# Performance work log

Hardware: AMD Instinct MI355X
Metric: run time of the kernel (lower is better)

Reference implementation:

```python
import jax, jax.numpy as jnp
import numpy as np
import math

T, B = 512, 32
QD, SD, H, NH = 128, 256, 512, 8
NQ, NS, NSUB = 30000, 400, 8
DKEY = QD + 2 * SD      # 640
DVAL = 4 * SD + QD      # 1152
P = H + 2 * SD + QD     # 1152 (pred_in_feature)
DH = H // NH            # 64
NEG = -1e32


def _layernorm(x, g, b, eps=1e-5):
    mu = jnp.mean(x, axis=-1, keepdims=True)
    var = jnp.mean((x - mu) ** 2, axis=-1, keepdims=True)
    return (x - mu) * jax.lax.rsqrt(var + eps) * g + b


def setup_inputs() -> dict:
    key = jax.random.key(0)
    ks = iter(jax.random.split(key, 48))
    def nrm(shape, scale=0.05):
        return (scale * jax.random.normal(next(ks), shape)).astype(jnp.float32)
    inp = {}
    inp['ans'] = jax.random.randint(next(ks), (T, B), 1, 5, dtype=jnp.int32)
    inp['correct_ans'] = jax.random.randint(next(ks), (T, B), 1, 5, dtype=jnp.int32)
    inp['labels'] = jax.random.randint(next(ks), (T, B), 0, 2, dtype=jnp.int32)
    inp['mask'] = jnp.ones((T, B), jnp.float32)
    inp['q_ids'] = jax.random.randint(next(ks), (T, B), 0, NQ, dtype=jnp.int32)
    inp['subject_ids'] = jax.random.randint(next(ks), (T, B, NSUB), 0, NS, dtype=jnp.int32)
    inp['subject_mask'] = (jax.random.uniform(next(ks), (T, B, NSUB)) < 0.7).astype(jnp.float32)
    inp['Eq'] = nrm((NQ, QD)); inp['Es'] = nrm((NS, SD))
    inp['Ea'] = nrm((4, SD)); inp['El'] = nrm((2, SD))
    inp['Wq'] = nrm((H, DKEY)); inp['bq'] = jnp.zeros((H,), jnp.float32)
    inp['Wk'] = nrm((H, DKEY)); inp['bk'] = jnp.zeros((H,), jnp.float32)
    inp['Wv'] = nrm((H, DVAL)); inp['bv'] = jnp.zeros((H,), jnp.float32)
    inp['Wo'] = nrm((H, H)); inp['bo'] = jnp.zeros((H,), jnp.float32)
    inp['ln1_g'] = jnp.ones((H,), jnp.float32); inp['ln1_b'] = jnp.zeros((H,), jnp.float32)
    inp['W1'] = nrm((H, H)); inp['b1'] = jnp.zeros((H,), jnp.float32)
    inp['W2'] = nrm((H, H)); inp['b2'] = jnp.zeros((H,), jnp.float32)
    inp['ln2_g'] = jnp.ones((H,), jnp.float32); inp['ln2_b'] = jnp.zeros((H,), jnp.float32)
    inp['gammas'] = jnp.zeros((NH, 1, 1), jnp.float32)
    inp['L1W'] = nrm((P, P)); inp['L1b'] = jnp.zeros((P,), jnp.float32)
    inp['L2W'] = nrm((P, P)); inp['L2b'] = jnp.zeros((P,), jnp.float32)
    inp['OW'] = nrm((1, P)); inp['Ob'] = jnp.zeros((1,), jnp.float32)
    return inp


def _forward(ans, correct_ans, labels, q_ids, subject_ids,
             mask, subject_mask, Eq, Es, Ea, El,
             Wq, bq, Wk, bk, Wv, bv, Wo, bo, ln1_g, ln1_b,
             W1, b1, W2, b2, ln2_g, ln2_b, gammas,
             L1W, L1b, L2W, L2b, OW, Ob):
    m3 = mask[:, :, None]                                   # [T,B,1]
    subjects = jnp.sum(Es[subject_ids] * subject_mask[..., None], axis=2)   # [T,B,SD]
    questions = Eq[q_ids]                                   # [T,B,QD]
    ans_embed = Ea[ans - 1] * m3
    ca_embed = Ea[correct_ans - 1]
    lab_embed = El[labels] * m3
    query = jnp.concatenate([questions, subjects, ca_embed], axis=-1)       # [T,B,DKEY]
    value = jnp.concatenate([lab_embed, ans_embed, ca_embed, questions, subjects], axis=-1)  # [T,B,DVAL]
    # note: original applies q_linear to kk and k_linear to qq (qq==kk==query here); akt=True => no pos-embed
    q = (query @ Wq.T + bq).reshape(T, B, NH, DH).transpose(1, 2, 0, 3)     # [B,NH,T,DH]
    k = (query @ Wk.T + bk).reshape(T, B, NH, DH).transpose(1, 2, 0, 3)
    v = (value @ Wv.T + bv).reshape(T, B, NH, DH).transpose(1, 2, 0, 3)
    scores = jnp.einsum('bhqd,bhkd->bhqk', q, k) / math.sqrt(DH)            # [B,NH,T,T]
    scores = jnp.where(mask.T[:, None, None, :] == 0, NEG, scores)
    # exponential distance decay (Softplus-gamma), applied AFTER the key-pad fill as in the original
    idx = jnp.arange(T)
    pe = jnp.sqrt(jnp.abs(idx[None, :] - idx[:, None]).astype(jnp.float32)) # [T,T]
    total_effect = jnp.clip(jnp.exp(pe[None] * (-jax.nn.softplus(gammas))), 1e-5, 1e5)  # [NH,T,T]
    scores = scores * total_effect[None]
    causal_bad = jnp.triu(jnp.ones((T, T), bool))            # upper incl. diagonal is masked
    scores = jnp.where(causal_bad, NEG, scores)
    scores = jax.nn.softmax(scores, axis=-1)
    scores = scores.at[:, :, 0, :].set(0.0)                  # pad-zero first query row
    attn = jnp.einsum('bhqk,bhkd->bhqd', scores, v)
    concat = attn.transpose(2, 0, 1, 3).reshape(T, B, H)
    out = _layernorm(concat @ Wo.T + bo, ln1_g, ln1_b)
    ffn = jax.nn.relu(out @ W1.T + b1) @ W2.T + b2
    out = out + _layernorm(ffn, ln2_g, ln2_b)
    pred = jnp.concatenate([out, questions, subjects, ca_embed], axis=-1)   # [T,B,P]
    h = jax.nn.relu(pred @ L1W.T + L1b)
    h = jax.nn.relu(h @ L2W.T + L2b)
    logits = ((h + pred) @ OW.T + Ob)[..., 0]                # [T,B]
    y = labels.astype(jnp.float32)
    bce = jnp.maximum(logits, 0.0) - logits * y + jnp.log1p(jnp.exp(-jnp.abs(logits)))
    loss = jnp.mean(bce * mask) / jnp.mean(mask)
    return loss


def reference(ans, correct_ans, labels, mask, q_ids, subject_ids, subject_mask,
              Eq, Es, Ea, El, Wq, bq, Wk, bk, Wv, bv, Wo, bo, ln1_g, ln1_b,
              W1, b1, W2, b2, ln2_g, ln2_b, gammas, L1W, L1b, L2W, L2b, OW, Ob):
    return _forward(ans, correct_ans, labels, q_ids, subject_ids,
                    mask, subject_mask, Eq, Es, Ea, El,
                    Wq, bq, Wk, bk, Wv, bv, Wo, bo, ln1_g, ln1_b,
                    W1, b1, W2, b2, ln2_g, ln2_b, gammas,
                    L1W, L1b, L2W, L2b, OW, Ob)
```

## Files before the change

kernel.cpp:

```cpp
#include <hip/hip_runtime.h>
#include <math.h>

#define T_LEN 512
#define B_SZ  32
#define NHEAD 8
#define DHEAD 64
#define H_DIM 512
#define TBTOK 16384
#define P_DIM 1152

typedef unsigned short ushort_t;
typedef short short8 __attribute__((ext_vector_type(8)));
typedef float f32x4 __attribute__((ext_vector_type(4)));

__device__ __forceinline__ ushort_t f2bf(float f) {
    union { float f; unsigned int u; } v; v.f = f;
    unsigned int r = v.u + 0x7fffu + ((v.u >> 16) & 1u);
    return (ushort_t)(r >> 16);
}
__device__ __forceinline__ float bf2f(ushort_t h) {
    union { unsigned int u; float f; } v; v.u = ((unsigned int)h) << 16;
    return v.f;
}
__device__ __forceinline__ void gload_lds16(const void* g, void* l) {
    __builtin_amdgcn_global_load_lds(
        (const __attribute__((address_space(1))) void*)g,
        (__attribute__((address_space(3))) void*)l, 16, 0, 0);
}

__global__ __launch_bounds__(256) void convert_weights(
    const float* __restrict__ wq, const float* __restrict__ wk,
    const float* __restrict__ wv, const float* __restrict__ wo,
    const float* __restrict__ w1, const float* __restrict__ w2,
    const float* __restrict__ l1, const float* __restrict__ l2,
    ushort_t* __restrict__ dst, float* __restrict__ accum)
{
    if (blockIdx.x == 0 && threadIdx.x < 2) accum[threadIdx.x] = 0.f;
    const unsigned int offs[9] = {0u, 327680u, 655360u, 1245184u, 1507328u,
                                  1769472u, 2031616u, 3358720u, 4685824u};
    unsigned int c = (blockIdx.x * 256 + threadIdx.x) * 4;
    const float* srcs[8] = {wq, wk, wv, wo, w1, w2, l1, l2};
    int s = 0;
#pragma unroll
    for (int i = 0; i < 7; i++) s += (c >= offs[i + 1]) ? 1 : 0;
    float4 v = *(const float4*)(srcs[s] + (c - offs[s]));
    ushort4 o;
    o.x = f2bf(v.x); o.y = f2bf(v.y); o.z = f2bf(v.z); o.w = f2bf(v.w);
    *(ushort4*)(dst + c) = o;
}

__global__ __launch_bounds__(256) void embed_kernel(
    const int* __restrict__ ans, const int* __restrict__ cans,
    const int* __restrict__ labels, const float* __restrict__ mask,
    const int* __restrict__ qids, const int* __restrict__ sids,
    const float* __restrict__ smask,
    const float* __restrict__ Eq, const float* __restrict__ Es,
    const float* __restrict__ Ea, const float* __restrict__ El,
    ushort_t* __restrict__ pred_bf, ushort_t* __restrict__ value_bf,
    const float* __restrict__ OW, const float* __restrict__ Ob,
    float* __restrict__ lgits)
{
    __shared__ float red[4];
    int m = blockIdx.x;
    int tid = threadIdx.x;
    float mval = mask[m];
    int qid = qids[m];
    int a   = ans[m] - 1;
    int ca  = cans[m] - 1;
    int lb  = labels[m];
    ushort_t* pr = pred_bf  + (size_t)m * P_DIM;
    ushort_t* vr = value_bf + (size_t)m * P_DIM;

    float part = 0.f;
    if (tid < 128) {
        ushort_t qv = f2bf(Eq[(size_t)qid * 128 + tid]);
        pr[512 + tid] = qv;
        vr[768 + tid] = qv;
        part = bf2f(qv) * OW[512 + tid];
    }
    int d = tid;
    float s = 0.f;
#pragma unroll
    for (int j = 0; j < 8; j++) {
        int  sid = sids[m * 8 + j];
        float sm = smask[m * 8 + j];
        s += Es[(size_t)sid * 256 + d] * sm;
    }
    ushort_t sb = f2bf(s);
    pr[640 + d] = sb;
    vr[896 + d] = sb;
    ushort_t cab = f2bf(Ea[ca * 256 + d]);
    pr[896 + d] = cab;
    vr[512 + d] = cab;
    vr[256 + d] = f2bf(Ea[a * 256 + d] * mval);
    vr[0   + d] = f2bf(El[lb * 256 + d] * mval);

    part = fmaf(bf2f(sb),  OW[640 + d], part);
    part = fmaf(bf2f(cab), OW[896 + d], part);
#pragma unroll
    for (int off = 32; off >= 1; off >>= 1) part += __shfl_xor(part, off, 64);
    if ((tid & 63) == 0) red[tid >> 6] = part;
    __syncthreads();
    if (tid == 0) lgits[m] = red[0] + red[1] + red[2] + red[3] + Ob[0];
}

template<int MODE, bool RELU>
__global__ __launch_bounds__(256) void mgemm(
    const ushort_t* __restrict__ A, int lda,
    const ushort_t* __restrict__ W, int ldw,
    const float* __restrict__ bias, const float* __restrict__ bias2,
    ushort_t* __restrict__ Cb, ushort_t* __restrict__ Cb2, int ldc, int K,
    const float* __restrict__ OW, float* __restrict__ lg)
{
    __shared__ __align__(16) ushort_t As[128 * 32];
    __shared__ __align__(16) ushort_t Ws[128 * 32];
    __shared__ __align__(16) ushort_t et[4][32][72];

    const int m0 = blockIdx.x * 128;
    const int n0 = blockIdx.y * 128;
    const int tid  = threadIdx.x;
    const int wave = tid >> 6;
    const int lane = tid & 63;
    const int wm = wave & 1, wn = wave >> 1;

    f32x4 acc[4][4] = {};

    const int srow = lane >> 2;
    const int lchunk = ((((lane & 3) - ((srow >> 1) & 3)) & 3)) * 8;
    int arowA, arowB;
    if (MODE == 4) {
        int mA = m0 + wave * 32 + srow;
        int mB = mA + 16;
        arowA = ((mA & 511) << 5) + (mA >> 9);
        arowB = ((mB & 511) << 5) + (mB >> 9);
    } else {
        arowA = m0 + wave * 32 + srow;
        arowB = arowA + 16;
    }
    const ushort_t* Ag0 = A + (size_t)arowA * lda + lchunk;
    const ushort_t* Ag1 = A + (size_t)arowB * lda + lchunk;
    const ushort_t* Wg0 = W + (size_t)(n0 + wave * 32 + srow) * ldw + lchunk;
    const ushort_t* Wg1 = Wg0 + (size_t)16 * ldw;
    ushort_t* Al0 = &As[(wave * 32) * 32];
    ushort_t* Al1 = &As[(wave * 32 + 16) * 32];
    ushort_t* Wl0 = &Ws[(wave * 32) * 32];
    ushort_t* Wl1 = &Ws[(wave * 32 + 16) * 32];

    const int fr   = lane & 15;
    const int quad = lane >> 4;
    const int csw  = ((quad + ((fr >> 1) & 3)) & 3) * 8;

    for (int k0 = 0; k0 < K; k0 += 32) {
        gload_lds16(Ag0 + k0, Al0);
        gload_lds16(Ag1 + k0, Al1);
        gload_lds16(Wg0 + k0, Wl0);
        gload_lds16(Wg1 + k0, Wl1);
        __syncthreads();
        short8 af[4], wf[4];
#pragma unroll
        for (int i = 0; i < 4; i++)
            af[i] = *(const short8*)&As[(wm * 64 + i * 16 + fr) * 32 + csw];
#pragma unroll
        for (int j = 0; j < 4; j++)
            wf[j] = *(const short8*)&Ws[(wn * 64 + j * 16 + fr) * 32 + csw];
#pragma unroll
        for (int i = 0; i < 4; i++)
#pragma unroll
            for (int j = 0; j < 4; j++)
                acc[i][j] = __builtin_amdgcn_mfma_f32_16x16x32_bf16(
                    af[i], wf[j], acc[i][j], 0, 0, 0);
        __syncthreads();
    }

    if (MODE == 3) {
#pragma unroll
        for (int i = 0; i < 4; i++)
#pragma unroll
            for (int r = 0; r < 4; r++) {
                int row = m0 + wm * 64 + i * 16 + quad * 4 + r;
                float part = 0.f;
#pragma unroll
                for (int j = 0; j < 4; j++) {
                    int col = n0 + wn * 64 + j * 16 + fr;
                    float v = fmaxf(acc[i][j][r] + bias[col], 0.f);
                    part = fmaf(v, OW[col], part);
                }
                part += __shfl_xor(part, 1, 64);
                part += __shfl_xor(part, 2, 64);
                part += __shfl_xor(part, 4, 64);
                part += __shfl_xor(part, 8, 64);
                if (fr == 0) atomicAdd(&lg[row], part);
            }
        return;
    }

    const int nbase = n0 + wn * 64;
    bool side = (MODE == 5) && (nbase >= 512);
    const float* bp = side ? bias2 : bias;
    const int boff  = (MODE == 5) ? (nbase & 511) : nbase;
    const float scl = (MODE == 5 && !side) ? 0.125f : 1.f;

    const int sub8 = (lane & 7) * 8;
    const int grp  = lane >> 3;

#pragma unroll
    for (int hh = 0; hh < 2; hh++) {
        if (MODE == 4) {
#pragma unroll
            for (int i = 0; i < 4; i++)
#pragma unroll
                for (int r = 0; r < 4; r++) {
                    int rl = i * 16 + quad * 4 + r;
#pragma unroll
                    for (int j = 2 * hh; j < 2 * hh + 2; j++) {
                        int cl = j * 16 + fr;
                        float v = acc[i][j][r] + bp[boff + cl];
                        if (RELU) v = fmaxf(v, 0.f);
                        et[wave][cl - 32 * hh][rl] = f2bf(v);
                    }
                }
        } else {
#pragma unroll
            for (int i = 2 * hh; i < 2 * hh + 2; i++)
#pragma unroll
                for (int r = 0; r < 4; r++) {
                    int rl = i * 16 + quad * 4 + r;
#pragma unroll
                    for (int j = 0; j < 4; j++) {
                        int cl = j * 16 + fr;
                        float v = (acc[i][j][r] + bp[boff + cl]) * scl;
                        if (RELU) v = fmaxf(v, 0.f);
                        et[wave][rl - 32 * hh][cl] = f2bf(v);
                    }
                }
        }
#pragma unroll
        for (int rr = 0; rr < 4; rr++) {
            int rowl = rr * 8 + grp;
            short8 val = *(const short8*)&et[wave][rowl][sub8];
            if (MODE == 1) {
                int row = m0 + wm * 64 + 32 * hh + rowl;
                int col = nbase + sub8;
                *(short8*)&Cb[(size_t)row * ldc + col] = val;
            } else if (MODE == 5) {
                int row = m0 + wm * 64 + 32 * hh + rowl;
                int t = row >> 5, b = row & 31;
                int h = (nbase >> 6) & 7;
                ushort_t* base = side ? Cb2 : Cb;
                *(short8*)&base[(((size_t)(b * 8 + h)) << 15) + ((size_t)t << 6) + sub8] = val;
            } else {
                int m = m0 + wm * 64 + sub8;
                int b = m >> 9, t = m & 511;
                int h = nbase >> 6;
                int d = 32 * hh + rowl;
                *(short8*)&Cb[(((size_t)(b * 8 + h)) << 15) + ((size_t)d << 9) + t] = val;
            }
        }
    }
}

__global__ __launch_bounds__(256) void attn_mfma(
    const ushort_t* __restrict__ qb, const ushort_t* __restrict__ kb,
    const ushort_t* __restrict__ vtb, const float* __restrict__ mask,
    const float* __restrict__ gammas, ushort_t* __restrict__ attnc)
{
    __shared__ __align__(16) ushort_t kbuf[2][64 * 64];
    __shared__ __align__(16) ushort_t vbuf[2][64 * 64];
    __shared__ __align__(16) ushort_t ps[4][16][72];
    __shared__ float decayF[512];
    __shared__ float mneg[512];

    const int bh  = blockIdx.x;
    const int b   = bh >> 3;
    const int h   = bh & 7;
    const int qt0 = (7 - blockIdx.y) * 64;
    const int tid  = threadIdx.x;
    const int wave = tid >> 6;
    const int lane = tid & 63;
    const int fr   = lane & 15;
    const int quad = lane >> 4;

    {
        float g  = gammas[h];
        float sp = (g > 20.f) ? g : log1pf(expf(g));
        for (int i = tid; i < 512; i += 256) {
            decayF[i] = fmaxf(exp2f(-sp * 1.44269504f * sqrtf((float)i)), 1e-5f)
                        * 1.44269504f;
            mneg[i]   = (mask[(size_t)i * B_SZ + b] == 0.f) ? -1e32f : 0.f;
        }
    }

    const int qr0 = qt0 + wave * 16;
    const ushort_t* qbase = qb  + ((size_t)bh << 15);
    const ushort_t* kbase = kb  + ((size_t)bh << 15);
    const ushort_t* vbase = vtb + ((size_t)bh << 15);

    short8 af0 = *(const short8*)(qbase + (size_t)(qr0 + fr) * 64 + quad * 8);
    short8 af1 = *(const short8*)(qbase + (size_t)(qr0 + fr) * 64 + 32 + quad * 8);
    const short8 ones = {0x3F80, 0x3F80, 0x3F80, 0x3F80,
                         0x3F80, 0x3F80, 0x3F80, 0x3F80};

    const int rl0 = wave * 16 + (lane >> 3);
    const int rl1 = rl0 + 8;
    const int sc0 = (((lane & 7) - rl0) & 7) * 8;
    const int sc1 = (((lane & 7) - rl1) & 7) * 8;

    auto stage = [&](int kt, int bufi) {
        gload_lds16(kbase + (size_t)(kt + rl0) * 64 + sc0, &kbuf[bufi][(wave * 16) * 64]);
        gload_lds16(kbase + (size_t)(kt + rl1) * 64 + sc1, &kbuf[bufi][(wave * 16 + 8) * 64]);
        gload_lds16(vbase + (size_t)rl0 * T_LEN + kt + sc0, &vbuf[bufi][(wave * 16) * 64]);
        gload_lds16(vbase + (size_t)rl1 * T_LEN + kt + sc1, &vbuf[bufi][(wave * 16 + 8) * 64]);
    };
    auto frag = [&](const ushort_t* buf, int row, int lchunk) -> short8 {
        return *(const short8*)&buf[row * 64 + ((lchunk + row) & 7) * 8];
    };

    stage(0, 0);

    f32x4 o[4] = {};
    f32x4 lacc = {};
    int bufi = 0;

    for (int kt0 = 0; kt0 <= qt0; kt0 += 64) {
        __syncthreads();
        if (kt0 < qt0) stage(kt0 + 64, bufi ^ 1);
        const bool diag = (kt0 == qt0);
        const ushort_t* kb_ = kbuf[bufi];
        const ushort_t* vb_ = vbuf[bufi];

        f32x4 sacc[4] = {};
#pragma unroll
        for (int j = 0; j < 4; j++) {
            int row = j * 16 + fr;
            short8 k0 = frag(kb_, row, quad);
            short8 k1 = frag(kb_, row, quad + 4);
            sacc[j] = __builtin_amdgcn_mfma_f32_16x16x32_bf16(af0, k0, sacc[j], 0, 0, 0);
            sacc[j] = __builtin_amdgcn_mfma_f32_16x16x32_bf16(af1, k1, sacc[j], 0, 0, 0);
        }

#pragma unroll
        for (int j = 0; j < 4; j++) {
            int kg = kt0 + j * 16 + fr;
            float mn = mneg[kg];
            int qgb = qr0 + quad * 4;
            if (!diag) {
                int base = qgb - kg;
#pragma unroll
                for (int r = 0; r < 4; r++) {
                    float t = fmaf(sacc[j][r], decayF[base + r], mn);
                    union { float f; unsigned u; } cv; cv.f = exp2f(t);
                    ps[wave][quad * 4 + r][j * 16 + fr] = (ushort_t)(cv.u >> 16);
                }
            } else {
#pragma unroll
                for (int r = 0; r < 4; r++) {
                    int didx = qgb + r - kg;
                    float dec = decayF[didx > 0 ? didx : 0];
                    float t = fmaf(sacc[j][r], dec, mn);
                    if (didx <= 0) t = -1e32f;
                    union { float f; unsigned u; } cv; cv.f = exp2f(t);
                    ps[wave][quad * 4 + r][j * 16 + fr] = (ushort_t)(cv.u >> 16);
                }
            }
        }
        short8 pf0 = *(const short8*)&ps[wave][fr][quad * 8];
        short8 pf1 = *(const short8*)&ps[wave][fr][32 + quad * 8];
        lacc = __builtin_amdgcn_mfma_f32_16x16x32_bf16(pf0, ones, lacc, 0, 0, 0);
        lacc = __builtin_amdgcn_mfma_f32_16x16x32_bf16(pf1, ones, lacc, 0, 0, 0);
#pragma unroll
        for (int j2 = 0; j2 < 4; j2++) {
            int row = j2 * 16 + fr;
            short8 v0 = frag(vb_, row, quad);
            short8 v1 = frag(vb_, row, quad + 4);
            o[j2] = __builtin_amdgcn_mfma_f32_16x16x32_bf16(pf0, v0, o[j2], 0, 0, 0);
            o[j2] = __builtin_amdgcn_mfma_f32_16x16x32_bf16(pf1, v1, o[j2], 0, 0, 0);
        }
        bufi ^= 1;
    }

#pragma unroll
    for (int r = 0; r < 4; r++) {
        int qg = qr0 + quad * 4 + r;
        float linv = (qg == 0) ? 0.f : 1.f / lacc[r];
#pragma unroll
        for (int j2 = 0; j2 < 4; j2++)
            ps[wave][quad * 4 + r][j2 * 16 + fr] = f2bf(o[j2][r] * linv);
    }
    const int sub8 = (lane & 7) * 8;
    const int grp  = lane >> 3;
#pragma unroll
    for (int half = 0; half < 2; half++) {
        int rowl = half * 8 + grp;
        short8 val = *(const short8*)&ps[wave][rowl][sub8];
        int qg = qr0 + rowl;
        *(short8*)&attnc[((size_t)qg * B_SZ + b) * H_DIM + h * DHEAD + sub8] = val;
    }
}

__global__ __launch_bounds__(256) void ln1_kernel(
    const ushort_t* __restrict__ X, const float* __restrict__ g,
    const float* __restrict__ bta, ushort_t* __restrict__ Yb)
{
    int m    = blockIdx.x * 4 + (threadIdx.x >> 6);
    int lane = threadIdx.x & 63;
    int c0   = lane * 8;
    const ushort_t* xr = X + (size_t)m * H_DIM + c0;
    float x[8];
    float s = 0.f, ss = 0.f;
    short8 xv = *(const short8*)xr;
#pragma unroll
    for (int i = 0; i < 8; i++) {
        x[i] = bf2f((ushort_t)xv[i]);
        s += x[i]; ss += x[i] * x[i];
    }
#pragma unroll
    for (int off = 32; off >= 1; off >>= 1) {
        s  += __shfl_xor(s,  off, 64);
        ss += __shfl_xor(ss, off, 64);
    }
    float mu  = s * (1.f / 512.f);
    float var = ss * (1.f / 512.f) - mu * mu;
    float rs  = rsqrtf(var + 1e-5f);
    ushort_t yb[8];
#pragma unroll
    for (int i = 0; i < 8; i++)
        yb[i] = f2bf((x[i] - mu) * rs * g[c0 + i] + bta[c0 + i]);
    *(short8*)(Yb + (size_t)m * H_DIM + c0) = *(short8*)&yb[0];
}

__global__ __launch_bounds__(256) void ln2_kernel(
    const ushort_t* __restrict__ X, const float* __restrict__ g,
    const float* __restrict__ bta, const ushort_t* __restrict__ res,
    ushort_t* __restrict__ pred_bf, const float* __restrict__ OW,
    float* __restrict__ lg)
{
    int m    = blockIdx.x * 4 + (threadIdx.x >> 6);
    int lane = threadIdx.x & 63;
    int c0   = lane * 8;
    const ushort_t* xr = X + (size_t)m * H_DIM + c0;
    float x[8];
    float s = 0.f, ss = 0.f;
    short8 xv = *(const short8*)xr;
#pragma unroll
    for (int i = 0; i < 8; i++) {
        x[i] = bf2f((ushort_t)xv[i]);
        s += x[i]; ss += x[i] * x[i];
    }
#pragma unroll
    for (int off = 32; off >= 1; off >>= 1) {
        s  += __shfl_xor(s,  off, 64);
        ss += __shfl_xor(ss, off, 64);
    }
    float mu  = s * (1.f / 512.f);
    float var = ss * (1.f / 512.f) - mu * mu;
    float rs  = rsqrtf(var + 1e-5f);
    short8 rv = *(const short8*)(res + (size_t)m * H_DIM + c0);
    ushort_t yb[8];
    float part = 0.f;
#pragma unroll
    for (int i = 0; i < 8; i++) {
        float v = (x[i] - mu) * rs * g[c0 + i] + bta[c0 + i] + bf2f((ushort_t)rv[i]);
        yb[i] = f2bf(v);
        part = fmaf(v, OW[c0 + i], part);
    }
    *(short8*)(pred_bf + (size_t)m * P_DIM + c0) = *(short8*)&yb[0];
#pragma unroll
    for (int off = 32; off >= 1; off >>= 1) part += __shfl_xor(part, off, 64);
    if (lane == 0) lg[m] += part;
}

__global__ __launch_bounds__(256) void bce_kernel(
    const float* __restrict__ lg, const int* __restrict__ labels,
    const float* __restrict__ mask, float* __restrict__ accum)
{
    int m    = blockIdx.x * 256 + threadIdx.x;
    int lane = threadIdx.x & 63;
    float l  = lg[m];
    float y  = (float)labels[m];
    float mv = mask[m];
    float a  = (fmaxf(l, 0.f) - l * y + log1pf(expf(-fabsf(l)))) * mv;
#pragma unroll
    for (int off = 32; off >= 1; off >>= 1) {
        a  += __shfl_xor(a,  off, 64);
        mv += __shfl_xor(mv, off, 64);
    }
    if (lane == 0) {
        atomicAdd(accum,     a);
        atomicAdd(accum + 1, mv);
    }
}

__global__ void finalize_kernel(const float* __restrict__ accum, float* __restrict__ out)
{
    out[0] = accum[0] / accum[1];
}

extern "C" void kernel_launch(void* const* d_in, const int* in_sizes, int n_in,
                              void* d_out, int out_size, void* d_ws, size_t ws_size,
                              hipStream_t stream)
{
    (void)in_sizes; (void)n_in; (void)out_size;
    const int*   ans    = (const int*)  d_in[0];
    const int*   cans   = (const int*)  d_in[1];
    const int*   labels = (const int*)  d_in[2];
    const float* mask   = (const float*)d_in[3];
    const int*   qids   = (const int*)  d_in[4];
    const int*   sids   = (const int*)  d_in[5];
    const float* smask  = (const float*)d_in[6];
    const float* Eq     = (const float*)d_in[7];
    const float* Es     = (const float*)d_in[8];
    const float* Ea     = (const float*)d_in[9];
    const float* El     = (const float*)d_in[10];
    const float* Wq     = (const float*)d_in[11];
    const float* bq     = (const float*)d_in[12];
    const float* Wk     = (const float*)d_in[13];
    const float* bk     = (const float*)d_in[14];
    const float* Wv     = (const float*)d_in[15];
    const float* bv     = (const float*)d_in[16];
    const float* Wo     = (const float*)d_in[17];
    const float* bo     = (const float*)d_in[18];
    const float* ln1_g  = (const float*)d_in[19];
    const float* ln1_b  = (const float*)d_in[20];
    const float* W1     = (const float*)d_in[21];
    const float* b1     = (const float*)d_in[22];
    const float* W2     = (const float*)d_in[23];
    const float* b2     = (const float*)d_in[24];
    const float* ln2_g  = (const float*)d_in[25];
    const float* ln2_b  = (const float*)d_in[26];
    const float* gammas = (const float*)d_in[27];
    const float* L1W    = (const float*)d_in[28];
    const float* L1b    = (const float*)d_in[29];
    const float* L2W    = (const float*)d_in[30];
    const float* L2b    = (const float*)d_in[31];
    const float* OW     = (const float*)d_in[32];
    const float* Ob     = (const float*)d_in[33];
    float* out = (float*)d_out;

    const size_t U = (size_t)TBTOK * 64;
    if (ws_size < 42 * U * sizeof(float)) return;
    float* ws = (float*)d_ws;
    ushort_t* wtb      = (ushort_t*)(ws);
    ushort_t* pred_bf  = (ushort_t*)(ws + 3 * U);
    ushort_t* value_bf = (ushort_t*)(ws + 12 * U);
    ushort_t* qb       = (ushort_t*)(ws + 21 * U);
    ushort_t* kb       = (ushort_t*)(ws + 25 * U);
    ushort_t* vtb      = (ushort_t*)(ws + 29 * U);
    ushort_t* attnc_bf = (ushort_t*)(ws + 33 * U);
    ushort_t* x1_bf    = (ushort_t*)(ws + 12 * U);
    ushort_t* out1_bf  = (ushort_t*)(ws + 24 * U);
    ushort_t* f1_bf    = (ushort_t*)(ws + 28 * U);
    ushort_t* f2_bf    = (ushort_t*)(ws + 32 * U);
    ushort_t* h1_bf    = (ushort_t*)(ws + 12 * U);
    float*    lgits    = ws + 41 * U;
    float*    accum    = lgits + TBTOK;

    ushort_t* wqk_b = wtb + 0;
    ushort_t* wv_b  = wtb + 655360;
    ushort_t* wo_b  = wtb + 1245184;
    ushort_t* w1_b  = wtb + 1507328;
    ushort_t* w2_b  = wtb + 1769472;
    ushort_t* l1_b  = wtb + 2031616;
    ushort_t* l2_b  = wtb + 3358720;

    convert_weights<<<4576, 256, 0, stream>>>(Wq, Wk, Wv, Wo, W1, W2, L1W, L2W,
                                              wtb, accum);
    embed_kernel<<<TBTOK, 256, 0, stream>>>(ans, cans, labels, mask, qids, sids,
                                            smask, Eq, Es, Ea, El, pred_bf, value_bf,
                                            OW, Ob, lgits);
    mgemm<5,false><<<dim3(TBTOK/128, 8), 256, 0, stream>>>(
        pred_bf + 512, P_DIM, wqk_b, 640, bq, bk, qb, kb, 0, 640, nullptr, nullptr);
    mgemm<4,false><<<dim3(TBTOK/128, 4), 256, 0, stream>>>(
        value_bf, P_DIM, wv_b, P_DIM, bv, nullptr, vtb, nullptr, 0, P_DIM, nullptr, nullptr);
    attn_mfma<<<dim3(B_SZ * NHEAD, 8), 256, 0, stream>>>(
        qb, kb, vtb, mask, gammas, attnc_bf);
    mgemm<1,false><<<dim3(TBTOK/128, 4), 256, 0, stream>>>(
        attnc_bf, H_DIM, wo_b, H_DIM, bo, nullptr, x1_bf, nullptr, H_DIM, H_DIM, nullptr, nullptr);
    ln1_kernel<<<TBTOK/4, 256, 0, stream>>>(x1_bf, ln1_g, ln1_b, out1_bf);
    mgemm<1,true><<<dim3(TBTOK/128, 4), 256, 0, stream>>>(
        out1_bf, H_DIM, w1_b, H_DIM, b1, nullptr, f1_bf, nullptr, H_DIM, H_DIM, nullptr, nullptr);
    mgemm<1,false><<<dim3(TBTOK/128, 4), 256, 0, stream>>>(
        f1_bf, H_DIM, w2_b, H_DIM, b2, nullptr, f2_bf, nullptr, H_DIM, H_DIM, nullptr, nullptr);
    ln2_kernel<<<TBTOK/4, 256, 0, stream>>>(f2_bf, ln2_g, ln2_b, out1_bf, pred_bf, OW, lgits);
    mgemm<1,true><<<dim3(TBTOK/128, 9), 256, 0, stream>>>(
        pred_bf, P_DIM, l1_b, P_DIM, L1b, nullptr, h1_bf, nullptr, P_DIM, P_DIM, nullptr, nullptr);
    mgemm<3,true><<<dim3(TBTOK/128, 9), 256, 0, stream>>>(
        h1_bf, P_DIM, l2_b, P_DIM, L2b, nullptr, nullptr, nullptr, 0, P_DIM, OW, lgits);
    bce_kernel<<<TBTOK/256, 256, 0, stream>>>(lgits, labels, mask, accum);
    finalize_kernel<<<1, 1, 0, stream>>>(accum, out);
}
```

Measured before the change: 480.2 us.

## Use 256x256 pipelined GEMM for prediction MLP with padded weights

Adds a new 512-thread GEMM kernel with 256x256 output tiles, a double-buffered K pipeline split into half-steps, and priority hints around MFMA blocks. It is used for the two large prediction-MLP GEMMs (1152-wide). The L1/L2 weights, biases and OW are padded to 1280 rows/columns with zeros by a separate kernel so N divides into 256 tiles. This targets fewer redundant operand loads and better MFMA utilisation, at the cost of about 11% wasted padded compute, a larger h1 buffer and an extra weight-prep launch.

Result: slower. 506.5 us (+5.5%).

```diff
diff --git a/kernel.cpp b/kernel.cpp
--- a/kernel.cpp
+++ b/kernel.cpp
@@ -8,6 +8,7 @@
 #define H_DIM 512
 #define TBTOK 16384
 #define P_DIM 1152
+#define P_PAD 1280
 
 typedef unsigned short ushort_t;
 typedef short short8 __attribute__((ext_vector_type(8)));
@@ -32,21 +33,57 @@
     const float* __restrict__ wq, const float* __restrict__ wk,
     const float* __restrict__ wv, const float* __restrict__ wo,
     const float* __restrict__ w1, const float* __restrict__ w2,
-    const float* __restrict__ l1, const float* __restrict__ l2,
     ushort_t* __restrict__ dst, float* __restrict__ accum)
 {
     if (blockIdx.x == 0 && threadIdx.x < 2) accum[threadIdx.x] = 0.f;
-    const unsigned int offs[9] = {0u, 327680u, 655360u, 1245184u, 1507328u,
-                                  1769472u, 2031616u, 3358720u, 4685824u};
+    const unsigned int offs[7] = {0u, 327680u, 655360u, 1245184u, 1507328u,
+                                  1769472u, 2031616u};
     unsigned int c = (blockIdx.x * 256 + threadIdx.x) * 4;
-    const float* srcs[8] = {wq, wk, wv, wo, w1, w2, l1, l2};
+    const float* srcs[6] = {wq, wk, wv, wo, w1, w2};
     int s = 0;
 #pragma unroll
-    for (int i = 0; i < 7; i++) s += (c >= offs[i + 1]) ? 1 : 0;
+    for (int i = 0; i < 5; i++) s += (c >= offs[i + 1]) ? 1 : 0;
     float4 v = *(const float4*)(srcs[s] + (c - offs[s]));
     ushort4 o;
     o.x = f2bf(v.x); o.y = f2bf(v.y); o.z = f2bf(v.z); o.w = f2bf(v.w);
     *(ushort4*)(dst + c) = o;
+}
+
+__global__ __launch_bounds__(256) void pad_weights(
+    const float* __restrict__ l1, const float* __restrict__ l2,
+    const float* __restrict__ L1b, const float* __restrict__ L2b,
+    const float* __restrict__ OW,
+    ushort_t* __restrict__ l1d, ushort_t* __restrict__ l2d,
+    float* __restrict__ L1bp, float* __restrict__ L2bp, float* __restrict__ OWp)
+{
+    int blk = blockIdx.x;
+    if (blk < 1440) {
+        int o4 = (blk * 256 + threadIdx.x) * 4;
+        int row = o4 / 1152;
+        int col = o4 - row * 1152;
+        ushort4 o; o.x = 0; o.y = 0; o.z = 0; o.w = 0;
+        if (row < 1152) {
+            float4 v = *(const float4*)(l1 + (size_t)row * 1152 + col);
+            o.x = f2bf(v.x); o.y = f2bf(v.y); o.z = f2bf(v.z); o.w = f2bf(v.w);
+        }
+        *(ushort4*)(l1d + o4) = o;
+    } else if (blk < 3040) {
+        int o4 = ((blk - 1440) * 256 + threadIdx.x) * 4;
+        int row = o4 / 1280;
+        int col = o4 - row * 1280;
+        ushort4 o; o.x = 0; o.y = 0; o.z = 0; o.w = 0;
+        if (row < 1152 && col < 1152) {
+            float4 v = *(const float4*)(l2 + (size_t)row * 1152 + col);
+            o.x = f2bf(v.x); o.y = f2bf(v.y); o.z = f2bf(v.z); o.w = f2bf(v.w);
+        }
+        *(ushort4*)(l2d + o4) = o;
+    } else {
+        for (int i = threadIdx.x; i < P_PAD; i += 256) {
+            L1bp[i] = (i < P_DIM) ? L1b[i] : 0.f;
+            L2bp[i] = (i < P_DIM) ? L2b[i] : 0.f;
+            OWp[i]  = (i < P_DIM) ? OW[i]  : 0.f;
+        }
+    }
 }
 
 __global__ __launch_bounds__(256) void embed_kernel(
@@ -170,28 +207,6 @@
                 acc[i][j] = __builtin_amdgcn_mfma_f32_16x16x32_bf16(
                     af[i], wf[j], acc[i][j], 0, 0, 0);
         __syncthreads();
-    }
-
-    if (MODE == 3) {
-#pragma unroll
-        for (int i = 0; i < 4; i++)
-#pragma unroll
-            for (int r = 0; r < 4; r++) {
-                int row = m0 + wm * 64 + i * 16 + quad * 4 + r;
-                float part = 0.f;
-#pragma unroll
-                for (int j = 0; j < 4; j++) {
-                    int col = n0 + wn * 64 + j * 16 + fr;
-                    float v = fmaxf(acc[i][j][r] + bias[col], 0.f);
-                    part = fmaf(v, OW[col], part);
-                }
-                part += __shfl_xor(part, 1, 64);
-                part += __shfl_xor(part, 2, 64);
-                part += __shfl_xor(part, 4, 64);
-                part += __shfl_xor(part, 8, 64);
-                if (fr == 0) atomicAdd(&lg[row], part);
-            }
-        return;
     }
 
     const int nbase = n0 + wn * 64;
@@ -255,6 +270,177 @@
                 int d = 32 * hh + rowl;
                 *(short8*)&Cb[(((size_t)(b * 8 + h)) << 15) + ((size_t)d << 9) + t] = val;
             }
+        }
+    }
+}
+
+template<int MODE, bool RELU>
+__global__ __launch_bounds__(512) void gemm256(
+    const ushort_t* __restrict__ A, int lda,
+    const ushort_t* __restrict__ W, int ldw,
+    const float* __restrict__ bias,
+    ushort_t* __restrict__ Cb, int ldc, int K,
+    const float* __restrict__ OW, float* __restrict__ lg)
+{
+    __shared__ __align__(16) ushort_t AB[2][2][2][256 * 32];
+    __shared__ __align__(16) ushort_t et[8][16][72];
+
+    const int m0 = blockIdx.x * 256;
+    const int n0 = blockIdx.y * 256;
+    const int tid  = threadIdx.x;
+    const int wave = tid >> 6;
+    const int lane = tid & 63;
+    const int wm = wave >> 2, wn = wave & 3;
+    const int fr   = lane & 15;
+    const int quad = lane >> 4;
+    const int csw  = ((quad + fr) & 3) * 8;
+
+    const int srow = wave * 32 + (lane >> 2);
+    const int sc   = (((lane & 3) - srow) & 3) * 8;
+    const ushort_t* Asrc = A + (size_t)(m0 + srow) * lda + sc;
+    const ushort_t* Wsrc = W + (size_t)(n0 + srow) * ldw + sc;
+    const size_t ldaL = (size_t)16 * lda;
+    const size_t ldwL = (size_t)16 * ldw;
+    const int NT = K >> 6;
+
+    auto stA = [&](int t, int kh) {
+        ushort_t* d = &AB[0][t & 1][kh][(wave * 32) * 32];
+        const ushort_t* s = Asrc + (size_t)(t * 64 + kh * 32);
+        gload_lds16(s, d);
+        gload_lds16(s + ldaL, d + 16 * 32);
+    };
+    auto stB = [&](int t, int kh) {
+        ushort_t* d = &AB[1][t & 1][kh][(wave * 32) * 32];
+        const ushort_t* s = Wsrc + (size_t)(t * 64 + kh * 32);
+        gload_lds16(s, d);
+        gload_lds16(s + ldwL, d + 16 * 32);
+    };
+
+    f32x4 acc[8][4] = {};
+
+    stA(0, 0); stB(0, 0); stA(0, 1); stB(0, 1);
+    if (NT > 1) { stA(1, 0); stB(1, 0); }
+    asm volatile("s_waitcnt vmcnt(4)" ::: "memory");
+    __builtin_amdgcn_s_barrier();
+
+    short8 af[4], bf[4];
+    for (int t = 0; t < NT; ++t) {
+        const int db = t & 1;
+        const ushort_t* Ar0 = &AB[0][db][0][0];
+        const ushort_t* Br0 = &AB[1][db][0][0];
+        const ushort_t* Ar1 = &AB[0][db][1][0];
+        const ushort_t* Br1 = &AB[1][db][1][0];
+
+#pragma unroll
+        for (int i = 0; i < 4; i++)
+            af[i] = *(const short8*)&Ar0[(wm * 128 + i * 16 + fr) * 32 + csw];
+#pragma unroll
+        for (int j = 0; j < 4; j++)
+            bf[j] = *(const short8*)&Br0[(wn * 64 + j * 16 + fr) * 32 + csw];
+        if (t + 1 < NT) stA(t + 1, 1);
+        __builtin_amdgcn_s_barrier();
+        __builtin_amdgcn_s_setprio(1);
+#pragma unroll
+        for (int i = 0; i < 4; i++)
+#pragma unroll
+            for (int j = 0; j < 4; j++)
+                acc[i][j] = __builtin_amdgcn_mfma_f32_16x16x32_bf16(
+                    af[i], bf[j], acc[i][j], 0, 0, 0);
+        __builtin_amdgcn_s_setprio(0);
+        __builtin_amdgcn_s_barrier();
+
+#pragma unroll
+        for (int i = 0; i < 4; i++)
+            af[i] = *(const short8*)&Ar0[(wm * 128 + 64 + i * 16 + fr) * 32 + csw];
+        if (t + 1 < NT) stB(t + 1, 1);
+        __builtin_amdgcn_s_barrier();
+        __builtin_amdgcn_s_setprio(1);
+#pragma unroll
+        for (int i = 0; i < 4; i++)
+#pragma unroll
+            for (int j = 0; j < 4; j++)
+                acc[4 + i][j] = __builtin_amdgcn_mfma_f32_16x16x32_bf16(
+                    af[i], bf[j], acc[4 + i][j], 0, 0, 0);
+        __builtin_amdgcn_s_setprio(0);
+        __builtin_amdgcn_s_barrier();
+
+#pragma unroll
+        for (int i = 0; i < 4; i++)
+            af[i] = *(const short8*)&Ar1[(wm * 128 + i * 16 + fr) * 32 + csw];
+#pragma unroll
+        for (int j = 0; j < 4; j++)
+            bf[j] = *(const short8*)&Br1[(wn * 64 + j * 16 + fr) * 32 + csw];
+        if (t + 2 < NT) stA(t + 2, 0);
+        __builtin_amdgcn_s_barrier();
+        __builtin_amdgcn_s_setprio(1);
+#pragma unroll
+        for (int i = 0; i < 4; i++)
+#pragma unroll
+            for (int j = 0; j < 4; j++)
+                acc[i][j] = __builtin_amdgcn_mfma_f32_16x16x32_bf16(
+                    af[i], bf[j], acc[i][j], 0, 0, 0);
+        __builtin_amdgcn_s_setprio(0);
+        __builtin_amdgcn_s_barrier();
+
+#pragma unroll
+        for (int i = 0; i < 4; i++)
+            af[i] = *(const short8*)&Ar1[(wm * 128 + 64 + i * 16 + fr) * 32 + csw];
+        if (t + 2 < NT) stB(t + 2, 0);
+        asm volatile("s_waitcnt vmcnt(4)" ::: "memory");
+        __builtin_amdgcn_s_barrier();
+        __builtin_amdgcn_s_setprio(1);
+#pragma unroll
+        for (int i = 0; i < 4; i++)
+#pragma unroll
+            for (int j = 0; j < 4; j++)
+                acc[4 + i][j] = __builtin_amdgcn_mfma_f32_16x16x32_bf16(
+                    af[i], bf[j], acc[4 + i][j], 0, 0, 0);
+        __builtin_amdgcn_s_setprio(0);
+        __builtin_amdgcn_s_barrier();
+    }
+
+    const int nbase = n0 + wn * 64;
+
+    if (MODE == 3) {
+#pragma unroll
+        for (int ii = 0; ii < 8; ii++)
+#pragma unroll
+            for (int r = 0; r < 4; r++) {
+                int row = m0 + wm * 128 + (ii >> 2) * 64 + (ii & 3) * 16 + quad * 4 + r;
+                float part = 0.f;
+#pragma unroll
+                for (int j = 0; j < 4; j++) {
+                    int col = nbase + j * 16 + fr;
+                    float v = fmaxf(acc[ii][j][r] + bias[col], 0.f);
+                    part = fmaf(v, OW[col], part);
+                }
+                part += __shfl_xor(part, 1, 64);
+                part += __shfl_xor(part, 2, 64);
+                part += __shfl_xor(part, 4, 64);
+                part += __shfl_xor(part, 8, 64);
+                if (fr == 0) atomicAdd(&lg[row], part);
+            }
+        return;
+    }
+
+    const int sub8 = (lane & 7) * 8;
+    const int grp  = lane >> 3;
+#pragma unroll
+    for (int ii = 0; ii < 8; ii++) {
+#pragma unroll
+        for (int r = 0; r < 4; r++)
+#pragma unroll
+            for (int j = 0; j < 4; j++) {
+                float v = acc[ii][j][r] + bias[nbase + j * 16 + fr];
+                if (RELU) v = fmaxf(v, 0.f);
+                et[wave][quad * 4 + r][j * 16 + fr] = f2bf(v);
+            }
+#pragma unroll
+        for (int rr = 0; rr < 2; rr++) {
+            int rowl = rr * 8 + grp;
+            short8 val = *(const short8*)&et[wave][rowl][sub8];
+            int row = m0 + wm * 128 + (ii >> 2) * 64 + (ii & 3) * 16 + rowl;
+            *(short8*)&Cb[(size_t)row * ldc + nbase + sub8] = val;
         }
     }
 }
@@ -553,6 +739,9 @@
     ushort_t* h1_bf    = (ushort_t*)(ws + 12 * U);
     float*    lgits    = ws + 41 * U;
     float*    accum    = lgits + TBTOK;
+    float*    OWp      = accum + 2;
+    float*    L1bp     = OWp + P_PAD;
+    float*    L2bp     = L1bp + P_PAD;
 
     ushort_t* wqk_b = wtb + 0;
     ushort_t* wv_b  = wtb + 655360;
@@ -560,10 +749,11 @@
     ushort_t* w1_b  = wtb + 1507328;
     ushort_t* w2_b  = wtb + 1769472;
     ushort_t* l1_b  = wtb + 2031616;
-    ushort_t* l2_b  = wtb + 3358720;
-
-    convert_weights<<<4576, 256, 0, stream>>>(Wq, Wk, Wv, Wo, W1, W2, L1W, L2W,
-                                              wtb, accum);
+    ushort_t* l2_b  = wtb + 3506176;
+
+    convert_weights<<<1984, 256, 0, stream>>>(Wq, Wk, Wv, Wo, W1, W2, wtb, accum);
+    pad_weights<<<3041, 256, 0, stream>>>(L1W, L2W, L1b, L2b, OW,
+                                          l1_b, l2_b, L1bp, L2bp, OWp);
     embed_kernel<<<TBTOK, 256, 0, stream>>>(ans, cans, labels, mask, qids, sids,
                                             smask, Eq, Es, Ea, El, pred_bf, value_bf,
                                             OW, Ob, lgits);
@@ -581,10 +771,10 @@
     mgemm<1,false><<<dim3(TBTOK/128, 4), 256, 0, stream>>>(
         f1_bf, H_DIM, w2_b, H_DIM, b2, nullptr, f2_bf, nullptr, H_DIM, H_DIM, nullptr, nullptr);
     ln2_kernel<<<TBTOK/4, 256, 0, stream>>>(f2_bf, ln2_g, ln2_b, out1_bf, pred_bf, OW, lgits);
-    mgemm<1,true><<<dim3(TBTOK/128, 9), 256, 0, stream>>>(
-        pred_bf, P_DIM, l1_b, P_DIM, L1b, nullptr, h1_bf, nullptr, P_DIM, P_DIM, nullptr, nullptr);
-    mgemm<3,true><<<dim3(TBTOK/128, 9), 256, 0, stream>>>(
-        h1_bf, P_DIM, l2_b, P_DIM, L2b, nullptr, nullptr, nullptr, 0, P_DIM, OW, lgits);
+    gemm256<1,true><<<dim3(TBTOK/256, P_PAD/256), 512, 0, stream>>>(
+        pred_bf, P_DIM, l1_b, P_DIM, L1bp, h1_bf, P_PAD, P_DIM, nullptr, nullptr);
+    gemm256<3,true><<<dim3(TBTOK/256, P_PAD/256), 512, 0, stream>>>(
+        h1_bf, P_PAD, l2_b, P_PAD, L2bp, nullptr, 0, P_PAD, OWp, lgits);
     bce_kernel<<<TBTOK/256, 256, 0, stream>>>(lgits, labels, mask, accum);
     finalize_kernel<<<1, 1, 0, stream>>>(accum, out);
 }
```
